# Optimization experiments

Measured on AMD Instinct MI355X. Metric: run time of the kernel, lower is better.

The kernel has to match this reference:

```python
import jax, jax.numpy as jnp
import numpy as np

NUM_CLASSES = 80
IMG = 608.0
L_COORD, L_NOOBJ, L_CLS = 5.0, 0.5, 1.0
EPS = 1e-7
ANCHORS = jnp.array([[12,16],[19,36],[40,28],[36,75],[76,55],[72,146],
                     [142,110],[192,243],[459,401]], dtype=jnp.float32).reshape(3, 3, 2)


def _iou(b1, b2):
    # boxes in (cx, cy, w, h); broadcastable shapes [..., 4]
    b1x1 = b1[..., 0] - b1[..., 2] * 0.5; b1y1 = b1[..., 1] - b1[..., 3] * 0.5
    b1x2 = b1[..., 0] + b1[..., 2] * 0.5; b1y2 = b1[..., 1] + b1[..., 3] * 0.5
    b2x1 = b2[..., 0] - b2[..., 2] * 0.5; b2y1 = b2[..., 1] - b2[..., 3] * 0.5
    b2x2 = b2[..., 0] + b2[..., 2] * 0.5; b2y2 = b2[..., 1] + b2[..., 3] * 0.5
    iw = jnp.clip(jnp.minimum(b1x2, b2x2) - jnp.maximum(b1x1, b2x1), 0.0)
    ih = jnp.clip(jnp.minimum(b1y2, b2y2) - jnp.maximum(b1y1, b2y1), 0.0)
    inter = iw * ih
    union = (b1x2 - b1x1) * (b1y2 - b1y1) + (b2x2 - b2x1) * (b2y2 - b2y1) - inter + EPS
    return inter / union


def _scale_loss(pred, anchors, targets):
    # pred: [B, A, H, W, 5+C]; anchors: [A, 2] (pixels); targets: [B, T, 5+C]
    B, A, H, W, _ = pred.shape
    C = pred.shape[-1] - 5
    T = targets.shape[1]

    # ---- decode predictions (decodePredictionsStable) ----
    gy, gx = jnp.meshgrid(jnp.arange(H), jnp.arange(W), indexing='ij')
    grid = jnp.stack([gx, gy], axis=-1).astype(pred.dtype)          # [H, W, 2]
    xy = jax.nn.sigmoid(pred[..., :2])
    wh = jnp.clip(pred[..., 2:4], -10.0, 10.0)
    box_xy = jnp.clip((xy + grid) / jnp.array([W, H], dtype=pred.dtype), 0.0, 1.0)
    box_wh = jnp.clip(jnp.exp(wh) * anchors[None, :, None, None, :] / IMG, 0.0, 1.0)
    pbox = jnp.concatenate([box_xy, box_wh], axis=-1)               # [B,A,H,W,4]
    pconf = jax.nn.sigmoid(pred[..., 4])                            # [B,A,H,W]
    pcls = jax.nn.sigmoid(pred[..., 5:])                            # [B,A,H,W,C]

    # ---- build targets (buildTargetsStable, vectorized scatter) ----
    gtbox = jnp.clip(targets[..., :4], 0.0, 1.0)                    # [B,T,4]
    valid = targets[..., 4] > 0                                     # [B,T]
    gxi = jnp.clip((gtbox[..., 0] * W).astype(jnp.int32), 0, W - 1)
    gyi = jnp.clip((gtbox[..., 1] * H).astype(jnp.int32), 0, H - 1)
    abox = jnp.concatenate([jnp.full((A, 2), 0.5, dtype=pred.dtype), anchors / IMG], axis=-1)
    ious = _iou(abox[None, None, :, :], gtbox[:, :, None, :])       # [B,T,A]
    best = jnp.argmax(ious, axis=-1).astype(jnp.int32)              # first max == torch strict '>' loop
    bidx = jnp.broadcast_to(jnp.arange(B, dtype=jnp.int32)[:, None], (B, T))

    flat = ((bidx * A + best) * H + gyi) * W + gxi                  # [B,T]
    order = jnp.arange(B * T, dtype=jnp.int32).reshape(B, T)
    ncells = B * A * H * W
    winner = jnp.full((ncells,), -1, jnp.int32).at[jnp.where(valid, flat, ncells)].max(order, mode='drop')
    keep = valid & (winner[flat] == order)
    bw = jnp.where(keep, bidx, B)                                   # out-of-range -> dropped

    mask = jnp.zeros((B, A, H, W), pred.dtype).at[bw, best, gyi, gxi].set(1.0, mode='drop')
    tbox = jnp.zeros((B, A, H, W, 4), pred.dtype).at[bw, best, gyi, gxi].set(gtbox, mode='drop')
    tcls = jnp.zeros((B, A, H, W, C), pred.dtype).at[bw, best, gyi, gxi].set(targets[..., 5:5 + C], mode='drop')

    npos = jnp.sum(mask)
    nneg = jnp.asarray(mask.size, pred.dtype) - npos

    # ---- coordinate loss: mean(1 - IoU) over positives ----
    coord = jnp.where(npos > 0, jnp.sum((1.0 - _iou(pbox, tbox)) * mask) / jnp.maximum(npos, 1.0), 0.0)

    # ---- confidence loss: BCE sum/npos + lambdaNoObj * BCE sum/nneg ----
    p = jnp.clip(pconf, 1e-10, 1.0 - 1e-10)
    bce = -(mask * jnp.log(p) + (1.0 - mask) * jnp.log1p(-p))
    conf = jnp.sum(bce * mask) / jnp.maximum(npos, 1.0) \
         + L_NOOBJ * jnp.sum(bce * (1.0 - mask)) / jnp.maximum(nneg, 1.0)

    # ---- class loss: BCE mean over positive rows ----
    pc = jnp.clip(pcls, 1e-10, 1.0 - 1e-10)
    tc = jnp.clip(tcls, 0.0, 1.0)
    bcec = -(tc * jnp.log(pc) + (1.0 - tc) * jnp.log1p(-pc))
    cls = jnp.where(npos > 0, jnp.sum(bcec * mask[..., None]) / jnp.maximum(npos * C, 1.0), 0.0)

    return coord, conf, cls


def setup_inputs() -> dict:
    key = jax.random.key(0)
    k0, k1, k2, k3 = jax.random.split(key, 4)
    B, T, C = 16, 50, NUM_CLASSES
    pred0 = jax.random.normal(k0, (B, 3, 76, 76, 5 + C), dtype=jnp.float32)
    pred1 = jax.random.normal(k1, (B, 3, 38, 38, 5 + C), dtype=jnp.float32)
    pred2 = jax.random.normal(k2, (B, 3, 19, 19, 5 + C), dtype=jnp.float32)
    targets = jax.random.uniform(k3, (B, T, 5 + C), dtype=jnp.float32)
    return {"pred0": pred0, "pred1": pred1, "pred2": pred2, "targets": targets}


def reference(pred0, pred1, pred2, targets):
    coord = jnp.float32(0.0); conf = jnp.float32(0.0); cls = jnp.float32(0.0)
    for s, pred in enumerate((pred0, pred1, pred2)):
        c, cf, cl = _scale_loss(pred, ANCHORS[s], targets)
        coord = coord + c; conf = conf + cf; cls = cls + cl
    total = L_COORD * coord + conf + L_CLS * cls
    return total, coord, conf, cls
```

## Files before the change

### kernel.cpp

```cpp
#include <hip/hip_runtime.h>
#include <math.h>

#define BB   16
#define TT   50
#define NCLS 80
#define IMGF 608.0f

#define H0 76
#define H1 38
#define H2 19
#define N0 277248
#define N1 69312
#define N2 17328

#define C0 5891520
#define C1 1472880
#define C2 368220

#define POS_BLOCKS_PER_SCALE 200
#define NPOS_BLOCKS (3*POS_BLOCKS_PER_SCALE)

#define F4_PER_THREAD 30
#define F4_PER_BLOCK (256*F4_PER_THREAD)
#define NOB0 768
#define NOB1 192
#define NOB2 48
#define NOBT (NOB0+NOB1+NOB2)
#define NBLK (NOBT + NPOS_BLOCKS)

__constant__ float c_anchors[3][3][2] = {
    {{12.f,16.f},{19.f,36.f},{40.f,28.f}},
    {{36.f,75.f},{76.f,55.f},{72.f,146.f}},
    {{142.f,110.f},{192.f,243.f},{459.f,401.f}}};
__constant__ int c_H[3] = {H0, H1, H2};

__device__ __forceinline__ float sigmoidf_(float x) { return 1.0f / (1.0f + expf(-x)); }
__device__ __forceinline__ float clipf_(float x, float lo, float hi) {
    return fminf(fmaxf(x, lo), hi);
}

__device__ __forceinline__ float iou4(float ax, float ay, float aw, float ah,
                                      float bx, float by, float bw, float bh) {
    float ax1 = ax - aw * 0.5f, ay1 = ay - ah * 0.5f;
    float ax2 = ax + aw * 0.5f, ay2 = ay + ah * 0.5f;
    float bx1 = bx - bw * 0.5f, by1 = by - bh * 0.5f;
    float bx2 = bx + bw * 0.5f, by2 = by + bh * 0.5f;
    float iw = fmaxf(fminf(ax2, bx2) - fmaxf(ax1, bx1), 0.f);
    float ih = fmaxf(fminf(ay2, by2) - fmaxf(ay1, by1), 0.f);
    float inter = iw * ih;
    float uni = (ax2 - ax1) * (ay2 - ay1) + (bx2 - bx1) * (by2 - by1) - inter + 1e-7f;
    return inter / uni;
}

__device__ __forceinline__ int target_cell(const float* tr, int s, float& cx, float& cy,
                                           float& w, float& h, int& best, int& gxi, int& gyi) {
    float t4 = tr[4];
    if (!(t4 > 0.f)) return -1;
    cx = clipf_(tr[0], 0.f, 1.f);
    cy = clipf_(tr[1], 0.f, 1.f);
    w  = clipf_(tr[2], 0.f, 1.f);
    h  = clipf_(tr[3], 0.f, 1.f);
    best = 0;
    float bi = -1e30f;
    #pragma unroll
    for (int a = 0; a < 3; a++) {
        float aw = c_anchors[s][a][0] / IMGF;
        float ah = c_anchors[s][a][1] / IMGF;
        float v = iou4(0.5f, 0.5f, aw, ah, cx, cy, w, h);
        if (v > bi) { bi = v; best = a; }
    }
    int H = c_H[s];
    gxi = (int)(cx * (float)H); gxi = min(max(gxi, 0), H - 1);
    gyi = (int)(cy * (float)H); gyi = min(max(gyi, 0), H - 1);
    return 0;
}

__global__ __launch_bounds__(256) void k_main(const float* __restrict__ p0,
                                              const float* __restrict__ p1,
                                              const float* __restrict__ p2,
                                              const float* __restrict__ targets,
                                              float* __restrict__ noobj_part,
                                              float* __restrict__ pos_part) {
    int blk = blockIdx.x;
    int lane = threadIdx.x & 63;
    int wv = threadIdx.x >> 6;

    __shared__ float sm1[4];
    __shared__ float sm5[4][5];

    if (blk < NOBT) {
        const float4* pv; unsigned cnt; int rb;
        if (blk < NOB0)             { pv = (const float4*)p0; cnt = C0; rb = blk; }
        else if (blk < NOB0 + NOB1) { pv = (const float4*)p1; cnt = C1; rb = blk - NOB0; }
        else                        { pv = (const float4*)p2; cnt = C2; rb = blk - NOB0 - NOB1; }
        unsigned gbase = (unsigned)rb * F4_PER_BLOCK + threadIdx.x;

        float s = 0.f;
        #pragma unroll 1
        for (int c = 0; c < 6; c++) {
            float4 v[5];
            #pragma unroll
            for (int j = 0; j < 5; j++) {
                unsigned q = gbase + (c * 5 + j) * 256;
                v[j] = (q < cnt) ? pv[q] : make_float4(0.f, 0.f, 0.f, 0.f);
            }
            #pragma unroll
            for (int j = 0; j < 5; j++) {
                unsigned q = gbase + (c * 5 + j) * 256;
                if (q < cnt) {
                    unsigned m = (4u * q) % 85u;
                    if (m - 1u <= 3u) {
                        float4 vv = v[j];
                        float x = (m == 4u) ? vv.x : (m == 3u) ? vv.y
                                : (m == 2u) ? vv.z : vv.w;
                        float sp = fmaxf(x, 0.f) + __logf(1.f + __expf(-fabsf(x)));
                        s += fminf(sp, 23.02585093f);
                    }
                }
            }
        }
        #pragma unroll
        for (int off = 32; off > 0; off >>= 1) s += __shfl_xor(s, off, 64);
        if (lane == 0) sm1[wv] = s;
        __syncthreads();
        if (threadIdx.x == 0)
            noobj_part[blk] = sm1[0] + sm1[1] + sm1[2] + sm1[3];
    } else {
        int bp = blk - NOBT;
        int s = bp / POS_BLOCKS_PER_SCALE;
        int order = (bp % POS_BLOCKS_PER_SCALE) * 4 + wv;

        float v_coord = 0.f, v_obj = 0.f, v_noadj = 0.f, v_cls = 0.f, v_np = 0.f;

        int b = order / TT, t = order % TT;
        const float* tr = targets + order * 85;
        float cx, cy, w, h; int best, gxi, gyi;
        if (target_cell(tr, s, cx, cy, w, h, best, gxi, gyi) == 0) {
            int H = c_H[s];
            int flat = ((b * 3 + best) * H + gyi) * H + gxi;

            bool lost = false;
            int tp = t + 1 + lane;
            if (tp < TT) {
                const float* tr2 = targets + (b * TT + tp) * 85;
                float cx2, cy2, w2, h2; int best2, gxi2, gyi2;
                if (target_cell(tr2, s, cx2, cy2, w2, h2, best2, gxi2, gyi2) == 0) {
                    int flat2 = ((b * 3 + best2) * H + gyi2) * H + gxi2;
                    lost = (flat2 == flat);
                }
            }
            if (__ballot(lost) == 0ull) {
                const float* pred = (s == 0) ? p0 : (s == 1) ? p1 : p2;
                const float* pc = pred + (long long)flat * 85;

                float px = sigmoidf_(pc[0]);
                float py = sigmoidf_(pc[1]);
                float bx = clipf_((px + (float)gxi) / (float)H, 0.f, 1.f);
                float by = clipf_((py + (float)gyi) / (float)H, 0.f, 1.f);
                float aw = c_anchors[s][best][0], ah = c_anchors[s][best][1];
                float bwv = clipf_(expf(clipf_(pc[2], -10.f, 10.f)) * aw / IMGF, 0.f, 1.f);
                float bhv = clipf_(expf(clipf_(pc[3], -10.f, 10.f)) * ah / IMGF, 0.f, 1.f);
                float iou = iou4(bx, by, bwv, bhv, cx, cy, w, h);

                float p = clipf_(sigmoidf_(pc[4]), 1e-10f, 1.0f);

                float pcv = clipf_(sigmoidf_(pc[5 + lane]), 1e-10f, 1.0f);
                float tc  = clipf_(tr[5 + lane], 0.f, 1.f);
                float cl  = -(tc * logf(pcv) + (1.f - tc) * log1pf(-pcv));
                if (lane < NCLS - 64) {
                    float pcv2 = clipf_(sigmoidf_(pc[5 + 64 + lane]), 1e-10f, 1.0f);
                    float tc2  = clipf_(tr[5 + 64 + lane], 0.f, 1.f);
                    cl += -(tc2 * logf(pcv2) + (1.f - tc2) * log1pf(-pcv2));
                }
                #pragma unroll
                for (int off = 32; off > 0; off >>= 1) cl += __shfl_xor(cl, off, 64);

                v_coord = 1.f - iou;
                v_obj   = -logf(p);
                v_noadj = -log1pf(-p);
                v_cls   = cl;
                v_np    = 1.f;
            }
        }

        if (lane == 0) {
            sm5[wv][0] = v_coord; sm5[wv][1] = v_obj; sm5[wv][2] = v_noadj;
            sm5[wv][3] = v_cls;   sm5[wv][4] = v_np;
        }
        __syncthreads();
        if (threadIdx.x < 5) {
            pos_part[bp * 5 + threadIdx.x] =
                sm5[0][threadIdx.x] + sm5[1][threadIdx.x] +
                sm5[2][threadIdx.x] + sm5[3][threadIdx.x];
        }
    }
}

__global__ __launch_bounds__(256) void k_final(const float* __restrict__ noobj_part,
                                               const float* __restrict__ pos_part,
                                               float* __restrict__ out) {
    float n0 = 0.f, n1 = 0.f, n2 = 0.f;
    #pragma unroll
    for (int r = 0; r < 4; r++) {
        int i = threadIdx.x + r * 256;
        if (i < NOB0)                    n0 += noobj_part[i];
        else if (i < NOB0 + NOB1)        n1 += noobj_part[i];
        else if (i < NOBT)               n2 += noobj_part[i];
    }
    float ps[3][5] = {};
    for (int i = threadIdx.x; i < NPOS_BLOCKS; i += 256) {
        int s = i / POS_BLOCKS_PER_SCALE;
        #pragma unroll
        for (int q = 0; q < 5; q++) ps[s][q] += pos_part[i * 5 + q];
    }

    __shared__ float red[18][256];
    red[0][threadIdx.x] = n0;
    red[1][threadIdx.x] = n1;
    red[2][threadIdx.x] = n2;
    #pragma unroll
    for (int s = 0; s < 3; s++) {
        #pragma unroll
        for (int q = 0; q < 5; q++) red[3 + s * 5 + q][threadIdx.x] = ps[s][q];
    }
    __syncthreads();
    for (int off = 128; off > 0; off >>= 1) {
        if (threadIdx.x < off) {
            #pragma unroll
            for (int r = 0; r < 18; r++)
                red[r][threadIdx.x] += red[r][threadIdx.x + off];
        }
        __syncthreads();
    }
    if (threadIdx.x == 0) {
        const float ncell[3] = {(float)N0, (float)N1, (float)N2};
        float coord = 0.f, conf = 0.f, cls = 0.f;
        #pragma unroll
        for (int s = 0; s < 3; s++) {
            float noobjTot = red[s][0];
            float co    = red[3 + s * 5 + 0][0];
            float ob    = red[3 + s * 5 + 1][0];
            float noadj = red[3 + s * 5 + 2][0];
            float cl    = red[3 + s * 5 + 3][0];
            float npos  = red[3 + s * 5 + 4][0];
            float nneg = ncell[s] - npos;
            float dn = fmaxf(npos, 1.f);
            conf += ob / dn + 0.5f * (noobjTot - noadj) / fmaxf(nneg, 1.f);
            if (npos > 0.f) {
                coord += co / dn;
                cls   += cl / fmaxf(npos * (float)NCLS, 1.f);
            }
        }
        out[0] = 5.0f * coord + conf + 1.0f * cls;
        out[1] = coord;
        out[2] = conf;
        out[3] = cls;
    }
}

extern "C" void kernel_launch(void* const* d_in, const int* in_sizes, int n_in,
                              void* d_out, int out_size, void* d_ws, size_t ws_size,
                              hipStream_t stream) {
    const float* p0 = (const float*)d_in[0];
    const float* p1 = (const float*)d_in[1];
    const float* p2 = (const float*)d_in[2];
    const float* tg = (const float*)d_in[3];
    float* out = (float*)d_out;

    char* ws = (char*)d_ws;
    float* noobj_part = (float*)ws;
    float* pos_part   = (float*)(ws + 8192);

    k_main<<<NBLK, 256, 0, stream>>>(p0, p1, p2, tg, noobj_part, pos_part);
    k_final<<<1, 256, 0, stream>>>(noobj_part, pos_part, out);
}
```

Baseline: 175.6 us.

## Gather only objectness logits instead of streaming whole prediction tensors

The no-object term now reads one strided float per grid cell (offset 4 of each 85-float record) instead of streaming every float4 of the prediction tensors and filtering by modulo. This avoids moving and index-testing the full ~120 MB of predictions just to use one channel in 85. Block counts drop to two cells per thread, and the workspace offset and final reduction are adjusted to match. Strided 340-byte access wastes most of each cache line and loses coalescing, so the actual bytes saved depend on cache line and sector granularity.

```diff
diff --git a/kernel.cpp b/kernel.cpp
--- a/kernel.cpp
+++ b/kernel.cpp
@@ -12,20 +12,15 @@
 #define N0 277248
 #define N1 69312
 #define N2 17328
-
-#define C0 5891520
-#define C1 1472880
-#define C2 368220
+#define NTOT (N0+N1+N2)
+
+#define NB0 542
+#define NB1 136
+#define NB2 34
+#define NOBT (NB0+NB1+NB2)
 
 #define POS_BLOCKS_PER_SCALE 200
 #define NPOS_BLOCKS (3*POS_BLOCKS_PER_SCALE)
-
-#define F4_PER_THREAD 30
-#define F4_PER_BLOCK (256*F4_PER_THREAD)
-#define NOB0 768
-#define NOB1 192
-#define NOB2 48
-#define NOBT (NOB0+NOB1+NOB2)
 #define NBLK (NOBT + NPOS_BLOCKS)
 
 __constant__ float c_anchors[3][3][2] = {
@@ -89,35 +84,24 @@
     __shared__ float sm5[4][5];
 
     if (blk < NOBT) {
-        const float4* pv; unsigned cnt; int rb;
-        if (blk < NOB0)             { pv = (const float4*)p0; cnt = C0; rb = blk; }
-        else if (blk < NOB0 + NOB1) { pv = (const float4*)p1; cnt = C1; rb = blk - NOB0; }
-        else                        { pv = (const float4*)p2; cnt = C2; rb = blk - NOB0 - NOB1; }
-        unsigned gbase = (unsigned)rb * F4_PER_BLOCK + threadIdx.x;
+        const float* pv; unsigned n; int rb;
+        if (blk < NB0)            { pv = p0; n = N0; rb = blk; }
+        else if (blk < NB0 + NB1) { pv = p1; n = N1; rb = blk - NB0; }
+        else                      { pv = p2; n = N2; rb = blk - NB0 - NB1; }
+        unsigned base = (unsigned)rb * 512u + threadIdx.x;
+
+        unsigned g0 = base, g1 = base + 256u;
+        float x0 = (g0 < n) ? pv[g0 * 85u + 4u] : 0.f;
+        float x1 = (g1 < n) ? pv[g1 * 85u + 4u] : 0.f;
 
         float s = 0.f;
-        #pragma unroll 1
-        for (int c = 0; c < 6; c++) {
-            float4 v[5];
-            #pragma unroll
-            for (int j = 0; j < 5; j++) {
-                unsigned q = gbase + (c * 5 + j) * 256;
-                v[j] = (q < cnt) ? pv[q] : make_float4(0.f, 0.f, 0.f, 0.f);
-            }
-            #pragma unroll
-            for (int j = 0; j < 5; j++) {
-                unsigned q = gbase + (c * 5 + j) * 256;
-                if (q < cnt) {
-                    unsigned m = (4u * q) % 85u;
-                    if (m - 1u <= 3u) {
-                        float4 vv = v[j];
-                        float x = (m == 4u) ? vv.x : (m == 3u) ? vv.y
-                                : (m == 2u) ? vv.z : vv.w;
-                        float sp = fmaxf(x, 0.f) + __logf(1.f + __expf(-fabsf(x)));
-                        s += fminf(sp, 23.02585093f);
-                    }
-                }
-            }
+        if (g0 < n) {
+            float sp = fmaxf(x0, 0.f) + __logf(1.f + __expf(-fabsf(x0)));
+            s += fminf(sp, 23.02585093f);
+        }
+        if (g1 < n) {
+            float sp = fmaxf(x1, 0.f) + __logf(1.f + __expf(-fabsf(x1)));
+            s += fminf(sp, 23.02585093f);
         }
         #pragma unroll
         for (int off = 32; off > 0; off >>= 1) s += __shfl_xor(s, off, 64);
@@ -201,11 +185,11 @@
                                                float* __restrict__ out) {
     float n0 = 0.f, n1 = 0.f, n2 = 0.f;
     #pragma unroll
-    for (int r = 0; r < 4; r++) {
+    for (int r = 0; r < 3; r++) {
         int i = threadIdx.x + r * 256;
-        if (i < NOB0)                    n0 += noobj_part[i];
-        else if (i < NOB0 + NOB1)        n1 += noobj_part[i];
-        else if (i < NOBT)               n2 += noobj_part[i];
+        if (i < NB0)                 n0 += noobj_part[i];
+        else if (i < NB0 + NB1)      n1 += noobj_part[i];
+        else if (i < NOBT)           n2 += noobj_part[i];
     }
     float ps[3][5] = {};
     for (int i = threadIdx.x; i < NPOS_BLOCKS; i += 256) {
@@ -269,7 +253,7 @@
 
     char* ws = (char*)d_ws;
     float* noobj_part = (float*)ws;
-    float* pos_part   = (float*)(ws + 8192);
+    float* pos_part   = (float*)(ws + 4096);
 
     k_main<<<NBLK, 256, 0, stream>>>(p0, p1, p2, tg, noobj_part, pos_part);
     k_final<<<1, 256, 0, stream>>>(noobj_part, pos_part, out);
```

New measurement: 158.5 us. 9.7% less time.
